# Performance work log

Measured on AMD Instinct MI355X. Metric: run time of the kernel, lower is better.

The kernel has to match this reference:

```python
import jax, jax.numpy as jnp
import numpy as np

NUM_GRAPHS = 1024
EPS = 1e-5  # BatchNorm eps
NEG_SLOPE = 0.2  # GATConv leaky_relu slope


def _bn(x, g, b):
    # train-mode BatchNorm over node/graph axis (biased variance, as torch)
    mu = jnp.mean(x, axis=0)
    var = jnp.mean((x - mu) ** 2, axis=0)
    return (x - mu) * jax.lax.rsqrt(var + EPS) * g + b


def _prelu(x, a):
    return jnp.where(x > 0, x, a * x)


def _gat_layer(x, src, dst, W, a_src, a_dst, bias, n_nodes):
    # single-head GATConv (heads=1, concat=True), self-loops already in src/dst
    h = x @ W                                            # [N, C]
    e = jax.nn.leaky_relu(jnp.take(h @ a_src, src) + jnp.take(h @ a_dst, dst), NEG_SLOPE)  # [E]
    m = jax.ops.segment_max(e, dst, num_segments=n_nodes)
    ex = jnp.exp(e - jnp.take(m, dst))
    denom = jax.ops.segment_sum(ex, dst, num_segments=n_nodes)
    alpha = ex / (jnp.take(denom, dst) + 1e-16)          # softmax over in-edges of each target
    out = jax.ops.segment_sum(jnp.take(h, src, axis=0) * alpha[:, None], dst, num_segments=n_nodes)
    return out + bias


def setup_inputs() -> dict:
    key = jax.random.key(0)
    ks = jax.random.split(key, 16)
    N, E, F, H, C = 500_000, 8_000_000, 7, 8, 2

    def gl(k, shp, fan_in):
        return (jax.random.normal(k, shp, jnp.float32) / np.sqrt(fan_in)).astype(jnp.float32)

    return {
        "x": jax.random.normal(ks[0], (N, F), jnp.float32),
        "edge_index": jax.random.randint(ks[1], (2, E), 0, N, jnp.int32),
        "batch": jnp.sort(jax.random.randint(ks[2], (N,), 0, NUM_GRAPHS, jnp.int32)),
        "W1": gl(ks[3], (F, H), F), "as1": gl(ks[4], (H,), H), "ad1": gl(ks[5], (H,), H), "b1": jnp.zeros((H,), jnp.float32),
        "W2": gl(ks[6], (H, H), H), "as2": gl(ks[7], (H,), H), "ad2": gl(ks[8], (H,), H), "b2": jnp.zeros((H,), jnp.float32),
        "W3": gl(ks[9], (H, H), H), "as3": gl(ks[10], (H,), H), "ad3": gl(ks[11], (H,), H), "b3": jnp.zeros((H,), jnp.float32),
        "g1": jnp.ones((H,), jnp.float32), "be1": jnp.zeros((H,), jnp.float32),
        "g2": jnp.ones((H,), jnp.float32), "be2": jnp.zeros((H,), jnp.float32),
        "g3": jnp.ones((H,), jnp.float32), "be3": jnp.zeros((H,), jnp.float32),
        "a_gnn": jnp.float32(0.25),
        "Wjk": gl(ks[12], (3 * H, H), 3 * H), "bjk": jnp.zeros((H,), jnp.float32),
        "Wm1": gl(ks[13], (H, H), H), "bm1": jnp.zeros((H,), jnp.float32),
        "gm": jnp.ones((H,), jnp.float32), "bem": jnp.zeros((H,), jnp.float32),
        "a_mlp": jnp.float32(0.25),
        "Wm2": gl(ks[14], (H, C), H), "bm2": jnp.zeros((C,), jnp.float32),
    }


def reference(x, edge_index, batch,
              W1, as1, ad1, b1, W2, as2, ad2, b2, W3, as3, ad3, b3,
              g1, be1, g2, be2, g3, be3, a_gnn, Wjk, bjk,
              Wm1, bm1, gm, bem, a_mlp, Wm2, bm2):
    N = x.shape[0]
    loop = jnp.arange(N, dtype=edge_index.dtype)  # GATConv add_self_loops=True
    src = jnp.concatenate([edge_index[0], loop])
    dst = jnp.concatenate([edge_index[1], loop])
    # 3-layer GAT, each: conv -> BatchNorm -> PReLU (dropout omitted: eval)
    h1 = _prelu(_bn(_gat_layer(x, src, dst, W1, as1, ad1, b1, N), g1, be1), a_gnn)
    h2 = _prelu(_bn(_gat_layer(h1, src, dst, W2, as2, ad2, b2, N), g2, be2), a_gnn)
    h3 = _prelu(_bn(_gat_layer(h2, src, dst, W3, as3, ad3, b3, N), g3, be3), a_gnn)
    # JumpingKnowledge 'cat' + projection to out_channels
    h = jnp.concatenate([h1, h2, h3], axis=1) @ Wjk + bjk   # [N, 8]
    pooled = jax.ops.segment_sum(h, batch, num_segments=NUM_GRAPHS)  # global_add_pool [G, 8]
    m1 = _prelu(_bn(pooled @ Wm1 + bm1, gm, bem), a_mlp)    # MLP hidden
    return m1 @ Wm2 + bm2                                    # [G, 2] logits
```

## Files before the change

### kernel.cpp

```cpp
#include <hip/hip_runtime.h>

typedef unsigned short u16;
typedef unsigned int   u32;

#define EPSBN     1e-5f
#define NEG_SLOPE 0.2f
#define NGRAPH    1024
#define NPB       512
#define CHUNK     16384
#define BKCAP     11264
#define NTILE     8
#define SLOTS     1536


static __device__ __forceinline__ float bfl(const u16* __restrict__ p, int i){
    return __uint_as_float(((u32)p[i]) << 16);
}
static __device__ __forceinline__ float ldf(const void* __restrict__ p, int i, bool f32){
    return f32 ? ((const float*)p)[i] : bfl((const u16*)p, i);
}
static __device__ __forceinline__ u16 f2bf(float f){
    u32 u = __float_as_uint(f);
    return (u16)((u + 0x7fffu + ((u >> 16) & 1u)) >> 16);
}
static __device__ __forceinline__ void unpack8(uint4 pk, float* a){
    a[0] = __uint_as_float((pk.x & 0xffffu) << 16);
    a[1] = __uint_as_float( pk.x & 0xffff0000u);
    a[2] = __uint_as_float((pk.y & 0xffffu) << 16);
    a[3] = __uint_as_float( pk.y & 0xffff0000u);
    a[4] = __uint_as_float((pk.z & 0xffffu) << 16);
    a[5] = __uint_as_float( pk.z & 0xffff0000u);
    a[6] = __uint_as_float((pk.w & 0xffffu) << 16);
    a[7] = __uint_as_float( pk.w & 0xffff0000u);
}
static __device__ __forceinline__ uint4 pack8(const float* a){
    uint4 pk;
    pk.x = (u32)f2bf(a[0]) | ((u32)f2bf(a[1])<<16);
    pk.y = (u32)f2bf(a[2]) | ((u32)f2bf(a[3])<<16);
    pk.z = (u32)f2bf(a[4]) | ((u32)f2bf(a[5])<<16);
    pk.w = (u32)f2bf(a[6]) | ((u32)f2bf(a[7])<<16);
    return pk;
}

static __device__ __forceinline__ int wave_scan_incl(int x){
    int lane = threadIdx.x & 63;
    #pragma unroll
    for (int off = 1; off < 64; off <<= 1){
        int y = __shfl_up(x, off, 64);
        if (lane >= off) x += y;
    }
    return x;
}
static __device__ __forceinline__ int block_scan_incl(int x, int* wpart){
    int t = threadIdx.x, lane = t & 63, wv = t >> 6;
    int nw = blockDim.x >> 6;
    int ws = wave_scan_incl(x);
    __syncthreads();
    if (lane == 63) wpart[wv] = ws;
    __syncthreads();
    if (wv == 0){
        int p = (lane < nw) ? wpart[lane] : 0;
        p = wave_scan_incl(p);
        if (lane < nw) wpart[lane] = p;
    }
    __syncthreads();
    int base = wv ? wpart[wv-1] : 0;
    return base + ws;
}

__global__ void k_sniff(const u16* __restrict__ x, int* __restrict__ flag){
    int lane = threadIdx.x;
    bool hit = false;
    for (int i = lane; i < 128; i += 64){
        float v = bfl(x, i);
        if (!(fabsf(v) <= 1e6f)) hit = true;
    }
    unsigned long long m = __ballot(hit);
    if (lane == 0) flag[0] = (m != 0ull) ? 1 : 0;
}

__global__ __launch_bounds__(1024) void k_binsort(const int* __restrict__ src,
                                                  const int* __restrict__ dst,
                                                  u32* __restrict__ stage,
                                                  int* __restrict__ matL,
                                                  int E, int B){
    __shared__ u32 pr[CHUNK];
    __shared__ int h[2048];
    __shared__ int wpart[16];
    int c = blockIdx.x, t = threadIdx.x;
    int e0 = c << 14, e1 = min(e0 + CHUNK, E), cn = e1 - e0;
    for (int b = t; b < B; b += 1024) h[b] = 0;
    __syncthreads();
    for (int i = e0 + t; i < e1; i += 1024) atomicAdd(&h[dst[i] >> 9], 1);
    __syncthreads();
    int base = t << 1, run = 0, loc[2];
    #pragma unroll
    for (int j = 0; j < 2; j++){
        int b = base + j;
        int v = (b < B) ? h[b] : 0;
        loc[j] = run; run += v;
    }
    int incl = block_scan_incl(run, wpart);
    int bex = incl - run;
    __syncthreads();
    #pragma unroll
    for (int j = 0; j < 2; j++){
        int b = base + j;
        if (b < B) h[b] = bex + loc[j];
    }
    __syncthreads();
    int* mrow = matL + (size_t)c * (B+1);
    for (int b = t; b < B; b += 1024) mrow[b] = h[b];
    if (t == 0) mrow[B] = cn;
    __syncthreads();
    for (int i = e0 + t; i < e1; i += 1024){
        int d = dst[i];
        int b = d >> 9;
        int p = atomicAdd(&h[b], 1);
        pr[p] = ((u32)src[i] << 9) | (u32)(d & 511);
    }
    __syncthreads();
    u32* srow = stage + ((size_t)c << 14);
    for (int i = t; i < cn; i += 1024) srow[i] = pr[i];
}

__global__ __launch_bounds__(256) void k_mtrans(const int* __restrict__ matL,
                                                int* __restrict__ matT, int R, int C){
    __shared__ int tile[32][33];
    int tx = threadIdx.x & 31, ty = threadIdx.x >> 5;
    int c0 = blockIdx.x << 5, r0 = blockIdx.y << 5;
    for (int j = ty; j < 32; j += 8){
        int r = r0 + j, c = c0 + tx;
        if (r < C && c < R) tile[j][tx] = matL[(size_t)r*R + c];
    }
    __syncthreads();
    for (int j = ty; j < 32; j += 8){
        int cc = c0 + j, rr = r0 + tx;
        if (cc < R && rr < C) matT[(size_t)cc*C + rr] = tile[tx][j];
    }
}

__global__ __launch_bounds__(256) void k_bucketsum(const int* __restrict__ matT,
                                                   int* __restrict__ bb, int B, int NC){
    int b = blockIdx.x, t = threadIdx.x;
    __shared__ int s[256];
    int acc = 0;
    const int* r0 = matT + (size_t)b*NC;
    const int* r1 = matT + (size_t)(b+1)*NC;
    for (int c = t; c < NC; c += 256) acc += r1[c] - r0[c];
    s[t] = acc; __syncthreads();
    for (int off = 128; off > 0; off >>= 1){
        if (t < off) s[t] += s[t+off];
        __syncthreads();
    }
    if (t == 0) bb[b] = s[0];
}

__global__ __launch_bounds__(1024) void k_bktbase(int* __restrict__ bb, int B){
    __shared__ int wpart[16];
    int t = threadIdx.x;
    int v = (t < B) ? bb[t] : 0;
    int incl = block_scan_incl(v, wpart);
    if (t < B) bb[t] = incl - v;
    if (t == B-1) bb[B] = incl;
}

__global__ __launch_bounds__(1024) void k_bucket(const u32* __restrict__ stage,
                                                 const int* __restrict__ matT,
                                                 const int* __restrict__ bb,
                                                 int* __restrict__ tileOfs,
                                                 u32* __restrict__ csr,
                                                 int N, int B, int NC){
    __shared__ u32 pr[BKCAP];
    __shared__ int hist[4096];
    __shared__ int sc[1024];
    __shared__ int lofsA[512];
    __shared__ int wpart[16];
    int k = blockIdx.x, t = threadIdx.x;
    int n0 = k << 9, n1 = min(n0 + NPB, N), nn = n1 - n0;
    int cnt = 0, lofs = 0;
    if (t < NC){
        lofs = matT[(size_t)k*NC + t];
        cnt  = matT[(size_t)(k+1)*NC + t] - lofs;
    }
    if (t < 512) lofsA[t] = lofs;
    int incl1 = block_scan_incl(cnt, wpart);
    sc[t] = incl1;
    __syncthreads();
    int total = sc[1023];
    int ec    = min(total, BKCAP - nn);
    for (int pidx = t; pidx < ec; pidx += 1024){
        int lo = 0, hi = 511;
        while (lo < hi){ int mid = (lo + hi) >> 1; if (sc[mid] > pidx) hi = mid; else lo = mid + 1; }
        int segStart = lo ? sc[lo-1] : 0;
        pr[pidx] = stage[((size_t)lo << 14) + lofsA[lo] + (pidx - segStart)];
    }
    __syncthreads();
    for (int j = t; j < nn; j += 1024) pr[ec + j] = ((u32)(n0 + j) << 9) | (u32)j;
    int ecnt = ec + nn;
    for (int i = t; i < 4096; i += 1024) hist[i] = 0;
    __syncthreads();
    for (int i = t; i < ecnt; i += 1024){
        u32 pk = pr[i];
        int dl = pk & 511;
        int tile = min((int)(pk >> 9) >> 16, NTILE-1);
        atomicAdd(&hist[(tile << 9) + dl], 1);
    }
    __syncthreads();
    int base = t << 2, run = 0, loc[4];
    #pragma unroll
    for (int j = 0; j < 4; j++){ loc[j] = run; run += hist[base + j]; }
    int incl2 = block_scan_incl(run, wpart);
    int bex = incl2 - run;
    __syncthreads();
    #pragma unroll
    for (int j = 0; j < 4; j++) hist[base + j] = bex + loc[j];
    if ((t & 127) == 0) tileOfs[(size_t)k*9 + (t >> 7)] = bex;
    if (t == 0)         tileOfs[(size_t)k*9 + 8] = ecnt;
    __syncthreads();
    int wbase = bb[k] + n0;
    for (int i = t; i < ecnt; i += 1024){
        u32 pk = pr[i];
        int dl = pk & 511;
        int tile = min((int)(pk >> 9) >> 16, NTILE-1);
        int p = atomicAdd(&hist[(tile << 9) + dl], 1);
        csr[wbase + p] = pk;
    }
}

__global__ void k_transform(const uint4* __restrict__ actpk, const void* __restrict__ xraw,
                            const int* __restrict__ dflag, int fin,
                            const void* __restrict__ W, const void* __restrict__ adst,
                            const float* __restrict__ stats, const void* __restrict__ gamma,
                            const void* __restrict__ beta, const void* __restrict__ alpha,
                            uint4* __restrict__ hrec, float* __restrict__ hd, int n){
    const bool f32 = dflag[0] != 0;
    __shared__ float Wl[64], dl[8], scl[8], sft[8], alv;
    int t = threadIdx.x;
    if (t < 64)            Wl[t]   = (t < fin*8) ? ldf(W, t, f32) : 0.f;
    if (t >= 64 && t < 72) dl[t-64] = ldf(adst, t-64, f32);
    if (t == 80) alv = ldf(alpha, 0, f32);
    if (stats && t < 8){
        float invN = 1.f/(float)n;
        float mu  = stats[t]*invN;
        float var = fmaxf(stats[8+t]*invN - mu*mu, 0.f);
        float s   = ldf(gamma, t, f32)*rsqrtf(var + EPSBN);
        scl[t] = s; sft[t] = ldf(beta, t, f32) - mu*s;
    }
    __syncthreads();
    int i = blockIdx.x*blockDim.x + t;
    if (i >= n) return;
    float a[8];
    if (xraw){
        #pragma unroll
        for (int k=0;k<7;k++) a[k] = ldf(xraw, i*7 + k, f32);
        a[7] = 0.f;
    } else {
        unpack8(actpk[i], a);
        #pragma unroll
        for (int j=0;j<8;j++){
            float y = a[j]*scl[j] + sft[j];
            a[j] = (y > 0.f) ? y : alv*y;
        }
    }
    float h[8];
    #pragma unroll
    for (int j=0;j<8;j++){
        float acc = 0.f;
        #pragma unroll
        for (int k=0;k<8;k++) acc += a[k]*Wl[k*8+j];
        h[j] = acc;
    }
    float s2 = 0.f;
    #pragma unroll
    for (int j=0;j<8;j++) s2 += h[j]*dl[j];
    hd[i] = s2;
    hrec[i] = pack8(h);
}

__global__ __launch_bounds__(512) void k_aggregate(
        const u32* __restrict__ csr, const int* __restrict__ bb,
        const int* __restrict__ tileOfs,
        const uint4* __restrict__ hrec, const float* __restrict__ hd,
        const void* __restrict__ asrc, const int* __restrict__ dflag,
        uint4* __restrict__ act, float* __restrict__ partials, int n){
    const bool f32 = dflag[0] != 0;
    __shared__ u32 stg[5*SLOTS];
    __shared__ u16 bs[512], be[512];
    __shared__ float alS[8];
    __shared__ float sred[8][16];
    int k = blockIdx.x, t = threadIdx.x;
    int n0 = k << 9;
    int nn = min(NPB, n - n0);
    if (t < 8) alS[t] = ldf(asrc, t, f32);
    float hdv = (t < nn) ? hd[n0 + t] : 0.f;
    int e0 = bb[k] + n0;
    const int* tof = tileOfs + (size_t)k*9;
    __syncthreads();
    float al[8];
    #pragma unroll
    for (int j = 0; j < 8; j++) al[j] = alS[j];
    float acc[8] = {0,0,0,0,0,0,0,0};
    float den = 0.f;

    for (int ti = 0; ti < NTILE; ++ti){
        int s0 = tof[ti], s1 = tof[ti+1];
        for (int c0 = s0; c0 < s1; c0 += SLOTS){
            int L = min(SLOTS, s1 - c0);
            bs[t] = 0; be[t] = 0;
            __syncthreads();
            {
                u32 pk[3]; uint4 hv[3];
                #pragma unroll
                for (int j = 0; j < 3; j++){
                    int idx = min(t + (j << 9), L - 1);
                    pk[j] = csr[e0 + c0 + idx];
                }
                #pragma unroll
                for (int j = 0; j < 3; j++) hv[j] = hrec[pk[j] >> 9];
                #pragma unroll
                for (int j = 0; j < 3; j++){
                    int i = t + (j << 9);
                    if (i < L){
                        stg[0*SLOTS + i] = hv[j].x;
                        stg[1*SLOTS + i] = hv[j].y;
                        stg[2*SLOTS + i] = hv[j].z;
                        stg[3*SLOTS + i] = hv[j].w;
                        stg[4*SLOTS + i] = pk[j] & 511u;
                    }
                }
            }
            __syncthreads();
            for (int i = t; i < L; i += 512){
                int dl = (int)stg[4*SLOTS + i];
                if (i == 0){
                    bs[dl] = 0;
                } else {
                    int dp = (int)stg[4*SLOTS + i - 1];
                    if (dp != dl){ bs[dl] = (u16)i; be[dp] = (u16)i; }
                }
                if (i == L-1) be[dl] = (u16)L;
            }
            __syncthreads();
            {
                int p0 = bs[t], p1 = be[t];
                for (int p = p0; p < p1; ++p){
                    uint4 hv = make_uint4(stg[0*SLOTS + p], stg[1*SLOTS + p],
                                          stg[2*SLOTS + p], stg[3*SLOTS + p]);
                    float h[8]; unpack8(hv, h);
                    float e = hdv;
                    #pragma unroll
                    for (int q = 0; q < 8; q++) e += h[q]*al[q];
                    e = (e > 0.f) ? e : NEG_SLOPE*e;
                    float w = __expf(e);
                    den += w;
                    #pragma unroll
                    for (int q = 0; q < 8; q++) acc[q] += w*h[q];
                }
            }
            __syncthreads();
        }
    }

    float o[8] = {0,0,0,0,0,0,0,0};
    if (t < nn){
        float inv = 1.f/(den + 1e-16f);
        #pragma unroll
        for (int j = 0; j < 8; j++) o[j] = acc[j]*inv;
        act[n0 + t] = pack8(o);
    }
    float v[16];
    #pragma unroll
    for (int j=0;j<8;j++){ v[j]=o[j]; v[8+j]=o[j]*o[j]; }
    #pragma unroll
    for (int off=32; off>0; off>>=1){
        #pragma unroll
        for (int j=0;j<16;j++) v[j] += __shfl_down(v[j], off, 64);
    }
    int lane = t & 63, wv = t >> 6;
    if (lane == 0){
        #pragma unroll
        for (int j=0;j<16;j++) sred[wv][j] = v[j];
    }
    __syncthreads();
    if (t < 16){
        float tot = 0.f;
        #pragma unroll
        for (int w=0; w<8; w++) tot += sred[w][t];
        partials[(size_t)blockIdx.x*16 + t] = tot;
    }
}

__global__ void k_statreduce(const float* __restrict__ partials, float* __restrict__ stats, int nb){
    __shared__ float s[256];
    int t = threadIdx.x;
    int col = t & 15, rg = t >> 4;
    float acc = 0.f;
    for (int r = rg; r < nb; r += 16) acc += partials[(size_t)r*16 + col];
    s[t] = acc; __syncthreads();
    if (t < 16){
        float tot = 0.f;
        #pragma unroll
        for (int k=0;k<16;k++) tot += s[k*16 + t];
        stats[t] = tot;
    }
}

static __device__ __forceinline__ int lowerb(const int* __restrict__ a, int n, int key){
    int lo = 0, hi = n;
    while (lo < hi){ int mid = (lo + hi) >> 1; if (a[mid] < key) lo = mid + 1; else hi = mid; }
    return lo;
}

__global__ __launch_bounds__(256) void k_jkpool(
        const uint4* __restrict__ a1, const uint4* __restrict__ a2, const uint4* __restrict__ a3,
        const float* __restrict__ st1, const float* __restrict__ st2, const float* __restrict__ st3,
        const void* __restrict__ g1, const void* __restrict__ be1,
        const void* __restrict__ g2, const void* __restrict__ be2,
        const void* __restrict__ g3, const void* __restrict__ be3,
        const void* __restrict__ alpha,
        const void* __restrict__ Wjk, const void* __restrict__ bjk,
        const int* __restrict__ dflag,
        const int* __restrict__ batch, float* __restrict__ pooled, int n){
    const bool f32 = dflag[0] != 0;
    __shared__ float Wl[192], bl[8], scl[24], sft[24], alv;
    __shared__ int rng[2];
    int t = threadIdx.x, g = blockIdx.x;
    if (t < 192) Wl[t] = ldf(Wjk, t, f32);
    if (t < 8)   bl[t] = ldf(bjk, t, f32);
    if (t < 24){
        int L = t >> 3, j = t & 7;
        const float* st = (L==0)? st1 : (L==1)? st2 : st3;
        const void* gg  = (L==0)? g1  : (L==1)? g2  : g3;
        const void* bb_ = (L==0)? be1 : (L==1)? be2 : be3;
        float invN = 1.f/(float)n;
        float mu  = st[j]*invN;
        float var = fmaxf(st[8+j]*invN - mu*mu, 0.f);
        float s   = ldf(gg, j, f32)*rsqrtf(var + EPSBN);
        scl[t] = s; sft[t] = ldf(bb_, j, f32) - mu*s;
    }
    if (t == 30) alv = ldf(alpha, 0, f32);
    if (t == 0) rng[0] = lowerb(batch, n, g);
    if (t == 1) rng[1] = lowerb(batch, n, g+1);
    __syncthreads();
    int lo = rng[0], hi = rng[1];
    float pa[8] = {0,0,0,0,0,0,0,0};
    for (int i = lo + t; i < hi; i += 256){
        float c[24];
        unpack8(a1[i], c);
        unpack8(a2[i], c+8);
        unpack8(a3[i], c+16);
        #pragma unroll
        for (int k=0;k<24;k++){
            float y = c[k]*scl[k] + sft[k];
            c[k] = (y > 0.f) ? y : alv*y;
        }
        #pragma unroll
        for (int j=0;j<8;j++){
            float acc = bl[j];
            #pragma unroll
            for (int k=0;k<24;k++) acc += c[k]*Wl[k*8+j];
            pa[j] += acc;
        }
    }
    #pragma unroll
    for (int off=32; off>0; off>>=1){
        #pragma unroll
        for (int j=0;j<8;j++) pa[j] += __shfl_down(pa[j], off, 64);
    }
    __shared__ float sr[4][8];
    int lane = t & 63, wv = t >> 6;
    if (lane == 0){
        #pragma unroll
        for (int j=0;j<8;j++) sr[wv][j] = pa[j];
    }
    __syncthreads();
    if (t < 8){
        float tot = sr[0][t]+sr[1][t]+sr[2][t]+sr[3][t];
        pooled[(size_t)g*8 + t] = tot;
    }
}

__global__ __launch_bounds__(1024) void k_final(
        const float* __restrict__ pooled,
        const void* __restrict__ Wm1, const void* __restrict__ bm1,
        const void* __restrict__ gm, const void* __restrict__ bem,
        const void* __restrict__ am,
        const void* __restrict__ Wm2, const void* __restrict__ bm2,
        const int* __restrict__ dflag,
        float* __restrict__ out, int G){
    const bool f32 = dflag[0] != 0;
    int t = threadIdx.x;
    float tv[8] = {0,0,0,0,0,0,0,0};
    if (t < G){
        float r[8];
        #pragma unroll
        for (int j=0;j<8;j++) r[j] = pooled[(size_t)t*8+j];
        #pragma unroll
        for (int j=0;j<8;j++){
            float acc = ldf(bm1, j, f32);
            #pragma unroll
            for (int k=0;k<8;k++) acc += r[k]*ldf(Wm1, k*8+j, f32);
            tv[j] = acc;
        }
    }
    float v[16];
    #pragma unroll
    for (int j=0;j<8;j++){ v[j]=tv[j]; v[8+j]=tv[j]*tv[j]; }
    #pragma unroll
    for (int off=32; off>0; off>>=1){
        #pragma unroll
        for (int j=0;j<16;j++) v[j] += __shfl_down(v[j], off, 64);
    }
    __shared__ float sred[16][16];
    int lane = t & 63, wv = t >> 6;
    if (lane == 0){
        #pragma unroll
        for (int j=0;j<16;j++) sred[wv][j] = v[j];
    }
    __syncthreads();
    __shared__ float stt[16];
    if (t < 16){
        float tot = 0.f;
        #pragma unroll
        for (int w=0; w<16; w++) tot += sred[w][t];
        stt[t] = tot;
    }
    __syncthreads();
    if (t < G){
        float a = ldf(am, 0, f32);
        float invG = 1.f/(float)G;
        float m1[8];
        #pragma unroll
        for (int j=0;j<8;j++){
            float mu  = stt[j]*invG;
            float var = fmaxf(stt[8+j]*invG - mu*mu, 0.f);
            float y = (tv[j]-mu)*rsqrtf(var+EPSBN)*ldf(gm,j,f32)+ldf(bem,j,f32);
            m1[j] = (y>0.f)? y : a*y;
        }
        #pragma unroll
        for (int c=0;c<2;c++){
            float oacc = ldf(bm2, c, f32);
            #pragma unroll
            for (int k=0;k<8;k++) oacc += m1[k]*ldf(Wm2, k*2+c, f32);
            out[(size_t)t*2+c] = oacc;
        }
    }
}

extern "C" void kernel_launch(void* const* d_in, const int* in_sizes, int n_in,
                              void* d_out, int out_size, void* d_ws, size_t ws_size,
                              hipStream_t stream){
    const u16* x16   = (const u16*)d_in[0];
    const void* x    = d_in[0];
    const int* ei    = (const int*)d_in[1];
    const int* batch = (const int*)d_in[2];
    int N = in_sizes[2];
    int E = in_sizes[1] / 2;
    const int* srcA = ei;
    const int* dstA = ei + E;
    const void *W1=d_in[3],  *as1=d_in[4],  *ad1=d_in[5];
    const void *W2=d_in[7],  *as2=d_in[8],  *ad2=d_in[9];
    const void *W3=d_in[11], *as3=d_in[12], *ad3=d_in[13];
    const void *g1=d_in[15], *be1=d_in[16];
    const void *g2=d_in[17], *be2=d_in[18];
    const void *g3=d_in[19], *be3=d_in[20];
    const void *agnn=d_in[21];
    const void *Wjk=d_in[22], *bjk=d_in[23];
    const void *Wm1=d_in[24], *bm1=d_in[25];
    const void *gm =d_in[26], *bem=d_in[27];
    const void *amlp=d_in[28];
    const void *Wm2=d_in[29], *bm2=d_in[30];

    char* p = (char*)d_ws;
    auto carve = [&](size_t bytes) -> void* {
        void* r = (void*)p;
        p += (bytes + 255) & ~(size_t)255;
        return r;
    };
    size_t M = (size_t)E + (size_t)N;
    int nb512 = (N + 511)/512;
    int B  = (N + NPB - 1) / NPB;
    int NC = (E + CHUNK - 1) / CHUNK;
    int*   dflag  = (int*)  carve(256);
    int*   bb     = (int*)  carve(((size_t)B+1)*4);
    int*   tileOfs= (int*)  carve((size_t)B*9*4);
    int*   matL   = (int*)  carve((size_t)NC*(B+1)*4);
    int*   matT   = (int*)  carve((size_t)(B+1)*NC*4);
    u32*   stage  = (u32*)  carve((size_t)NC*CHUNK*4);
    u32*   csr    = (u32*)  carve(M*4);
    uint4* hrec   = (uint4*)carve((size_t)N*16);
    float* hd     = (float*)carve((size_t)N*4);
    uint4* act1   = (uint4*)carve((size_t)N*16);
    uint4* act2   = (uint4*)carve((size_t)N*16);
    uint4* act3   = (uint4*)carve((size_t)N*16);
    float* parts  = (float*)carve((size_t)nb512*64);
    float* stats1 = (float*)carve(64);
    float* stats2 = (float*)carve(64);
    float* stats3 = (float*)carve(64);
    float* pooled = (float*)carve((size_t)NGRAPH*32);
    (void)ws_size; (void)n_in;

    k_sniff<<<1, 64, 0, stream>>>(x16, dflag);

    k_binsort  <<<NC, 1024, 0, stream>>>(srcA, dstA, stage, matL, E, B);
    {
        dim3 tg(((B+1) + 31)/32, (NC + 31)/32);
        k_mtrans<<<tg, 256, 0, stream>>>(matL, matT, B+1, NC);
    }
    k_bucketsum<<<B, 256, 0, stream>>>(matT, bb, B, NC);
    k_bktbase  <<<1, 1024, 0, stream>>>(bb, B);
    k_bucket   <<<B, 1024, 0, stream>>>(stage, matT, bb, tileOfs, csr, N, B, NC);

    k_transform <<<nb512, 512, 0, stream>>>(nullptr, x, dflag, 7, W1, ad1,
                                            nullptr, nullptr, nullptr, agnn, hrec, hd, N);
    k_aggregate <<<B, 512, 0, stream>>>(csr, bb, tileOfs, hrec, hd, as1, dflag, act1, parts, N);
    k_statreduce<<<1, 256, 0, stream>>>(parts, stats1, nb512);
    k_transform <<<nb512, 512, 0, stream>>>(act1, nullptr, dflag, 8, W2, ad2,
                                            stats1, g1, be1, agnn, hrec, hd, N);
    k_aggregate <<<B, 512, 0, stream>>>(csr, bb, tileOfs, hrec, hd, as2, dflag, act2, parts, N);
    k_statreduce<<<1, 256, 0, stream>>>(parts, stats2, nb512);
    k_transform <<<nb512, 512, 0, stream>>>(act2, nullptr, dflag, 8, W3, ad3,
                                            stats2, g2, be2, agnn, hrec, hd, N);
    k_aggregate <<<B, 512, 0, stream>>>(csr, bb, tileOfs, hrec, hd, as3, dflag, act3, parts, N);
    k_statreduce<<<1, 256, 0, stream>>>(parts, stats3, nb512);

    k_jkpool<<<NGRAPH, 256, 0, stream>>>(act1, act2, act3, stats1, stats2, stats3,
                                         g1, be1, g2, be2, g3, be3, agnn,
                                         Wjk, bjk, dflag, batch, pooled, N);
    int G = out_size / 2;
    k_final <<<1, 1024, 0, stream>>>(pooled, Wm1, bm1, gm, bem, amlp, Wm2, bm2, dflag, (float*)d_out, G);
}
```

Before: 573.4 us.

## Prefetch next edge chunk during aggregation and fold BN stats via atomics

The aggregate kernel now software-pipelines its chunk loop. The csr entries and gathered hrec records for the next chunk are loaded into registers while the current chunk's segment boundaries and softmax accumulation run, so gather latency is hidden behind compute. Separately, the per-block BN partial sums are atomically added into a zeroed stats buffer (cleared in k_bktbase), which removes three k_statreduce launches. This costs extra registers, which may lower occupancy, and float atomics make the stats order nondeterministic.

```diff
diff --git a/kernel.cpp b/kernel.cpp
--- a/kernel.cpp
+++ b/kernel.cpp
@@ -156,9 +156,11 @@
     if (t == 0) bb[b] = s[0];
 }
 
-__global__ __launch_bounds__(1024) void k_bktbase(int* __restrict__ bb, int B){
+__global__ __launch_bounds__(1024) void k_bktbase(int* __restrict__ bb, int B,
+                                                  float* __restrict__ statsAll){
     __shared__ int wpart[16];
     int t = threadIdx.x;
+    if (t < 48) statsAll[t] = 0.f;
     int v = (t < B) ? bb[t] : 0;
     int incl = block_scan_incl(v, wpart);
     if (t < B) bb[t] = incl - v;
@@ -283,19 +285,20 @@
         const int* __restrict__ tileOfs,
         const uint4* __restrict__ hrec, const float* __restrict__ hd,
         const void* __restrict__ asrc, const int* __restrict__ dflag,
-        uint4* __restrict__ act, float* __restrict__ partials, int n){
+        uint4* __restrict__ act, float* __restrict__ stats, int n){
     const bool f32 = dflag[0] != 0;
     __shared__ u32 stg[5*SLOTS];
     __shared__ u16 bs[512], be[512];
     __shared__ float alS[8];
     __shared__ float sred[8][16];
+    __shared__ int tofS[9];
     int k = blockIdx.x, t = threadIdx.x;
     int n0 = k << 9;
     int nn = min(NPB, n - n0);
     if (t < 8) alS[t] = ldf(asrc, t, f32);
+    if (t < 9) tofS[t] = tileOfs[(size_t)k*9 + t];
     float hdv = (t < nn) ? hd[n0 + t] : 0.f;
     int e0 = bb[k] + n0;
-    const int* tof = tileOfs + (size_t)k*9;
     __syncthreads();
     float al[8];
     #pragma unroll
@@ -303,63 +306,71 @@
     float acc[8] = {0,0,0,0,0,0,0,0};
     float den = 0.f;
 
-    for (int ti = 0; ti < NTILE; ++ti){
-        int s0 = tof[ti], s1 = tof[ti+1];
-        for (int c0 = s0; c0 < s1; c0 += SLOTS){
-            int L = min(SLOTS, s1 - c0);
-            bs[t] = 0; be[t] = 0;
-            __syncthreads();
-            {
-                u32 pk[3]; uint4 hv[3];
+    int wt = 0, wc = 0;
+    while (wt < NTILE && wc >= tofS[wt+1]){ wt++; if (wt < NTILE) wc = tofS[wt]; }
+
+    u32 pkc[3]; uint4 hvc[3];
+    if (wt < NTILE){
+        int L = min(SLOTS, tofS[wt+1] - wc);
+        #pragma unroll
+        for (int j = 0; j < 3; j++) pkc[j] = csr[e0 + wc + min(t + (j << 9), L - 1)];
+        #pragma unroll
+        for (int j = 0; j < 3; j++) hvc[j] = hrec[pkc[j] >> 9];
+    }
+
+    while (wt < NTILE){
+        int L = min(SLOTS, tofS[wt+1] - wc);
+        __syncthreads();
+        #pragma unroll
+        for (int j = 0; j < 3; j++){
+            int i = t + (j << 9);
+            if (i < L){
+                stg[0*SLOTS + i] = hvc[j].x;
+                stg[1*SLOTS + i] = hvc[j].y;
+                stg[2*SLOTS + i] = hvc[j].z;
+                stg[3*SLOTS + i] = hvc[j].w;
+                stg[4*SLOTS + i] = pkc[j] & 511u;
+            }
+        }
+        bs[t] = 0; be[t] = 0;
+        __syncthreads();
+        int nwt = wt, nwc = wc + SLOTS;
+        while (nwt < NTILE && nwc >= tofS[nwt+1]){ nwt++; if (nwt < NTILE) nwc = tofS[nwt]; }
+        if (nwt < NTILE){
+            int Ln = min(SLOTS, tofS[nwt+1] - nwc);
+            #pragma unroll
+            for (int j = 0; j < 3; j++) pkc[j] = csr[e0 + nwc + min(t + (j << 9), Ln - 1)];
+            #pragma unroll
+            for (int j = 0; j < 3; j++) hvc[j] = hrec[pkc[j] >> 9];
+        }
+        for (int i = t; i < L; i += 512){
+            int dl = (int)stg[4*SLOTS + i];
+            if (i == 0){
+                bs[dl] = 0;
+            } else {
+                int dp = (int)stg[4*SLOTS + i - 1];
+                if (dp != dl){ bs[dl] = (u16)i; be[dp] = (u16)i; }
+            }
+            if (i == L-1) be[dl] = (u16)L;
+        }
+        __syncthreads();
+        {
+            int p0 = bs[t], p1 = be[t];
+            for (int p = p0; p < p1; ++p){
+                uint4 hv = make_uint4(stg[0*SLOTS + p], stg[1*SLOTS + p],
+                                      stg[2*SLOTS + p], stg[3*SLOTS + p]);
+                float h[8]; unpack8(hv, h);
+                float e = hdv;
                 #pragma unroll
-                for (int j = 0; j < 3; j++){
-                    int idx = min(t + (j << 9), L - 1);
-                    pk[j] = csr[e0 + c0 + idx];
-                }
+                for (int q = 0; q < 8; q++) e += h[q]*al[q];
+                e = (e > 0.f) ? e : NEG_SLOPE*e;
+                float w = __expf(e);
+                den += w;
                 #pragma unroll
-                for (int j = 0; j < 3; j++) hv[j] = hrec[pk[j] >> 9];
-                #pragma unroll
-                for (int j = 0; j < 3; j++){
-                    int i = t + (j << 9);
-                    if (i < L){
-                        stg[0*SLOTS + i] = hv[j].x;
-                        stg[1*SLOTS + i] = hv[j].y;
-                        stg[2*SLOTS + i] = hv[j].z;
-                        stg[3*SLOTS + i] = hv[j].w;
-                        stg[4*SLOTS + i] = pk[j] & 511u;
-                    }
-                }
+                for (int q = 0; q < 8; q++) acc[q] += w*h[q];
             }
-            __syncthreads();
-            for (int i = t; i < L; i += 512){
-                int dl = (int)stg[4*SLOTS + i];
-                if (i == 0){
-                    bs[dl] = 0;
-                } else {
-                    int dp = (int)stg[4*SLOTS + i - 1];
-                    if (dp != dl){ bs[dl] = (u16)i; be[dp] = (u16)i; }
-                }
-                if (i == L-1) be[dl] = (u16)L;
-            }
-            __syncthreads();
-            {
-                int p0 = bs[t], p1 = be[t];
-                for (int p = p0; p < p1; ++p){
-                    uint4 hv = make_uint4(stg[0*SLOTS + p], stg[1*SLOTS + p],
-                                          stg[2*SLOTS + p], stg[3*SLOTS + p]);
-                    float h[8]; unpack8(hv, h);
-                    float e = hdv;
-                    #pragma unroll
-                    for (int q = 0; q < 8; q++) e += h[q]*al[q];
-                    e = (e > 0.f) ? e : NEG_SLOPE*e;
-                    float w = __expf(e);
-                    den += w;
-                    #pragma unroll
-                    for (int q = 0; q < 8; q++) acc[q] += w*h[q];
-                }
-            }
-            __syncthreads();
-        }
+        }
+        wt = nwt; wc = nwc;
     }
 
     float o[8] = {0,0,0,0,0,0,0,0};
@@ -387,22 +398,7 @@
         float tot = 0.f;
         #pragma unroll
         for (int w=0; w<8; w++) tot += sred[w][t];
-        partials[(size_t)blockIdx.x*16 + t] = tot;
-    }
-}
-
-__global__ void k_statreduce(const float* __restrict__ partials, float* __restrict__ stats, int nb){
-    __shared__ float s[256];
-    int t = threadIdx.x;
-    int col = t & 15, rg = t >> 4;
-    float acc = 0.f;
-    for (int r = rg; r < nb; r += 16) acc += partials[(size_t)r*16 + col];
-    s[t] = acc; __syncthreads();
-    if (t < 16){
-        float tot = 0.f;
-        #pragma unroll
-        for (int k=0;k<16;k++) tot += s[k*16 + t];
-        stats[t] = tot;
+        atomicAdd(&stats[t], tot);
     }
 }
 
@@ -594,10 +590,10 @@
     uint4* act1   = (uint4*)carve((size_t)N*16);
     uint4* act2   = (uint4*)carve((size_t)N*16);
     uint4* act3   = (uint4*)carve((size_t)N*16);
-    float* parts  = (float*)carve((size_t)nb512*64);
-    float* stats1 = (float*)carve(64);
-    float* stats2 = (float*)carve(64);
-    float* stats3 = (float*)carve(64);
+    float* statsA = (float*)carve(256);
+    float* stats1 = statsA;
+    float* stats2 = statsA + 16;
+    float* stats3 = statsA + 32;
     float* pooled = (float*)carve((size_t)NGRAPH*32);
     (void)ws_size; (void)n_in;
 
@@ -609,21 +605,18 @@
         k_mtrans<<<tg, 256, 0, stream>>>(matL, matT, B+1, NC);
     }
     k_bucketsum<<<B, 256, 0, stream>>>(matT, bb, B, NC);
-    k_bktbase  <<<1, 1024, 0, stream>>>(bb, B);
+    k_bktbase  <<<1, 1024, 0, stream>>>(bb, B, statsA);
     k_bucket   <<<B, 1024, 0, stream>>>(stage, matT, bb, tileOfs, csr, N, B, NC);
 
     k_transform <<<nb512, 512, 0, stream>>>(nullptr, x, dflag, 7, W1, ad1,
                                             nullptr, nullptr, nullptr, agnn, hrec, hd, N);
-    k_aggregate <<<B, 512, 0, stream>>>(csr, bb, tileOfs, hrec, hd, as1, dflag, act1, parts, N);
-    k_statreduce<<<1, 256, 0, stream>>>(parts, stats1, nb512);
+    k_aggregate <<<B, 512, 0, stream>>>(csr, bb, tileOfs, hrec, hd, as1, dflag, act1, stats1, N);
     k_transform <<<nb512, 512, 0, stream>>>(act1, nullptr, dflag, 8, W2, ad2,
                                             stats1, g1, be1, agnn, hrec, hd, N);
-    k_aggregate <<<B, 512, 0, stream>>>(csr, bb, tileOfs, hrec, hd, as2, dflag, act2, parts, N);
-    k_statreduce<<<1, 256, 0, stream>>>(parts, stats2, nb512);
+    k_aggregate <<<B, 512, 0, stream>>>(csr, bb, tileOfs, hrec, hd, as2, dflag, act2, stats2, N);
     k_transform <<<nb512, 512, 0, stream>>>(act2, nullptr, dflag, 8, W3, ad3,
                                             stats2, g2, be2, agnn, hrec, hd, N);
-    k_aggregate <<<B, 512, 0, stream>>>(csr, bb, tileOfs, hrec, hd, as3, dflag, act3, parts, N);
-    k_statreduce<<<1, 256, 0, stream>>>(parts, stats3, nb512);
+    k_aggregate <<<B, 512, 0, stream>>>(csr, bb, tileOfs, hrec, hd, as3, dflag, act3, stats3, N);
 
     k_jkpool<<<NGRAPH, 256, 0, stream>>>(act1, act2, act3, stats1, stats2, stats3,
                                          g1, be1, g2, be2, g3, be3, agnn,
```

After: 525.0 us. 8.4% less time.
